# Kernel optimization log

Measured on AMD Instinct MI355X. Metric: run time of the kernel, lower is better.

## Reference

```python
import jax, jax.numpy as jnp
import numpy as np

B, T, C = 2, 2048, 2048
H, KVH, HD = 16, 4, 128  # heads, kv heads, head_dim
G = H // KVH             # GQA group size
THETA = 10000.0


def _rope_cos_sin(t, hd, dtype):
    inv_freq = 1.0 / (THETA ** (jnp.arange(0, hd, 2, dtype=jnp.float32) / hd))
    pos = jnp.arange(t, dtype=jnp.float32)
    freqs = pos[:, None] * inv_freq[None, :]          # [T, hd/2]
    emb = jnp.concatenate([freqs, freqs], axis=-1)    # [T, hd]
    return jnp.cos(emb).astype(dtype), jnp.sin(emb).astype(dtype)


def _rotate_half(x):
    x1, x2 = jnp.split(x, 2, axis=-1)
    return jnp.concatenate([-x2, x1], axis=-1)


def setup_inputs() -> dict:
    key = jax.random.key(0)
    ks = jax.random.split(key, 5)
    s_in = 1.0 / np.sqrt(C)
    return {
        "x": jax.random.normal(ks[0], (B, T, C), jnp.float32),
        "wq": jax.random.normal(ks[1], (C, H * HD), jnp.float32) * s_in,
        "bq": jnp.zeros((H * HD,), jnp.float32),
        "wk": jax.random.normal(ks[2], (C, KVH * HD), jnp.float32) * s_in,
        "bk": jnp.zeros((KVH * HD,), jnp.float32),
        "wv": jax.random.normal(ks[3], (C, KVH * HD), jnp.float32) * s_in,
        "bv": jnp.zeros((KVH * HD,), jnp.float32),
        "wo": jax.random.normal(ks[4], (H * HD, C), jnp.float32) * (1.0 / np.sqrt(H * HD)),
    }


def reference(x, wq, bq, wk, bk, wv, bv, wo):
    b, t, c = x.shape
    q = (x @ wq + bq).reshape(b, t, H, HD).transpose(0, 2, 1, 3)    # [B,H,T,hd]
    k = (x @ wk + bk).reshape(b, t, KVH, HD).transpose(0, 2, 1, 3)  # [B,KVH,T,hd]
    v = (x @ wv + bv).reshape(b, t, KVH, HD).transpose(0, 2, 1, 3)

    cos, sin = _rope_cos_sin(t, HD, x.dtype)  # [T,hd]
    q = q * cos + _rotate_half(q) * sin
    k = k * cos + _rotate_half(k) * sin

    # GQA: group query heads over kv heads
    qg = q.reshape(b, KVH, G, t, HD)
    scale = 1.0 / np.sqrt(HD)
    scores = jnp.einsum('bkgtd,bksd->bkgts', qg, k) * scale  # [B,KVH,G,T,T]
    causal = jnp.tril(jnp.ones((t, t), bool))
    scores = jnp.where(causal, scores, jnp.finfo(scores.dtype).min)
    attn = jax.nn.softmax(scores, axis=-1)
    out = jnp.einsum('bkgts,bksd->bkgtd', attn, v)            # [B,KVH,G,T,hd]
    out = out.reshape(b, H, t, HD).transpose(0, 2, 1, 3).reshape(b, t, H * HD)
    return out @ wo
```

## Files before the change

### kernel.cpp

```cpp
#include <hip/hip_runtime.h>
#include <hip/hip_bf16.h>
#include <math.h>

#define B_ 2
#define T_ 2048
#define C_ 2048
#define H_ 16
#define KVH_ 4
#define HD_ 128
#define G_ (H_ / KVH_)
#define MROWS (B_ * T_)
#define NQKV (H_ * HD_ + 2 * KVH_ * HD_)
#define KOFF (H_ * HD_)
#define VOFF (H_ * HD_ + KVH_ * HD_)
#define L2T (13.287712379549449f / 64.0f)

typedef __hip_bfloat16 bf16;
typedef short bf16x8 __attribute__((ext_vector_type(8)));
typedef short bf16x4 __attribute__((ext_vector_type(4)));
typedef float f32x4 __attribute__((ext_vector_type(4)));

__device__ __forceinline__ void gload_lds16(const void* g, void* l) {
  __builtin_amdgcn_global_load_lds(
      (const __attribute__((address_space(1))) unsigned int*)g,
      (__attribute__((address_space(3))) unsigned int*)l, 16, 0, 0);
}

static __device__ __forceinline__ f32x4 mfma32k(bf16x8 a, bf16x8 b, f32x4 c) {
  return __builtin_amdgcn_mfma_f32_16x16x32_bf16(a, b, c, 0, 0, 0);
}

static __device__ __forceinline__ f32x4 mfma16(bf16x4 a, bf16x4 b, f32x4 c) {
#if __has_builtin(__builtin_amdgcn_mfma_f32_16x16x16_bf16)
  return __builtin_amdgcn_mfma_f32_16x16x16_bf16(a, b, c, 0, 0, 0);
#else
  return __builtin_amdgcn_mfma_f32_16x16x16bf16_1k(a, b, c, 0, 0, 0);
#endif
}

static __device__ __forceinline__ short f2bf(float x) {
  unsigned u = __builtin_bit_cast(unsigned, x);
  u += 0x7FFFu + ((u >> 16) & 1u);
  return (short)(u >> 16);
}

static __device__ __forceinline__ float bfh2f(short h) {
  unsigned u = ((unsigned)(unsigned short)h) << 16;
  return __builtin_bit_cast(float, u);
}

static __device__ __forceinline__ float fexp2(float x) {
#if __has_builtin(__builtin_amdgcn_exp2f)
  return __builtin_amdgcn_exp2f(x);
#else
  return exp2f(x);
#endif
}

__global__ __launch_bounds__(256) void prep_kernel(
    const float* __restrict__ x, bf16* __restrict__ xb,
    const float* __restrict__ wq, const float* __restrict__ wk,
    const float* __restrict__ wv, bf16* __restrict__ wqkvT,
    const float* __restrict__ wo, bf16* __restrict__ woT,
    float2* __restrict__ tab) {
  __shared__ float t[32][33];
  int bid = blockIdx.x;
  if (bid < 8192) {
    const int i = (bid * 256 + threadIdx.x) * 4;
    float4 v = *(const float4*)(x + i);
    xb[i + 0] = __float2bfloat16(v.x);
    xb[i + 1] = __float2bfloat16(v.y);
    xb[i + 2] = __float2bfloat16(v.z);
    xb[i + 3] = __float2bfloat16(v.w);
    return;
  }
  bid -= 8192;
  if (bid < 6144) {
    const int tx = threadIdx.x & 31, ty = threadIdx.x >> 5;
    const int c0 = (bid % 96) * 32;
    const int r0 = (bid / 96) * 32;
    const float* src;
    int nn, ld;
    if (c0 < KOFF)      { src = wq; nn = c0;        ld = 2048; }
    else if (c0 < VOFF) { src = wk; nn = c0 - KOFF; ld = 512; }
    else                { src = wv; nn = c0 - VOFF; ld = 512; }
#pragma unroll
    for (int it = 0; it < 4; ++it)
      t[ty + 8 * it][tx] = src[(size_t)(r0 + ty + 8 * it) * ld + nn + tx];
    __syncthreads();
#pragma unroll
    for (int it = 0; it < 4; ++it)
      wqkvT[(size_t)(c0 + ty + 8 * it) * 2048 + r0 + tx] =
          __float2bfloat16(t[tx][ty + 8 * it]);
    return;
  }
  bid -= 6144;
  if (bid < 4096) {
    const int tx = threadIdx.x & 31, ty = threadIdx.x >> 5;
    const int c0 = (bid & 63) * 32;
    const int r0 = (bid >> 6) * 32;
#pragma unroll
    for (int it = 0; it < 4; ++it)
      t[ty + 8 * it][tx] = wo[(size_t)(r0 + ty + 8 * it) * 2048 + c0 + tx];
    __syncthreads();
#pragma unroll
    for (int it = 0; it < 4; ++it)
      woT[(size_t)(c0 + ty + 8 * it) * 2048 + r0 + tx] =
          __float2bfloat16(t[tx][ty + 8 * it]);
    return;
  }
  bid -= 4096;
  {
    const int idx = bid * 256 + threadIdx.x;
    const int tt = idx >> 6, i = idx & 63;
    const float invf = fexp2(-(float)i * L2T);
    float s, c;
    __sincosf((float)tt * invf, &s, &c);
    tab[idx] = make_float2(c, s);
  }
}

__global__ __launch_bounds__(256) void pack_kv(const bf16* __restrict__ qkv,
                                               bf16* __restrict__ kp,
                                               bf16* __restrict__ vp,
                                               const float2* __restrict__ tab) {
  const int pid = blockIdx.x;
  if (pid < 512) {
    const int tile = pid & 63;
    const int bk = pid >> 6;
    const int b = bk >> 2, kvh = bk & 3;
#pragma unroll
    for (int u = 0; u < 2; ++u) {
      const int t = threadIdx.x + u * 256;
      const int kc = t >> 6, L = t & 63;
      const int trow = tile * 32 + 16 * (kc >> 2) + (L & 15);
      const bf16* src = qkv + (size_t)(b * T_ + trow) * NQKV +
                        KOFF + kvh * HD_ + (kc & 3) * 32 + (L >> 4) * 8;
      bf16x8 vs = *(const bf16x8*)src;
      bf16x8 vpair = *(const bf16x8*)(src + (((kc & 2) == 0) ? 64 : -64));
      const float2* tp = tab + trow * 64 + (kc & 1) * 32 + (L >> 4) * 8;
      bf16x8 outv;
#pragma unroll
      for (int jj = 0; jj < 8; ++jj) {
        const float2 cs = tp[jj];
        const float a = bfh2f(vs[jj]), p = bfh2f(vpair[jj]);
        outv[jj] = f2bf(((kc & 2) == 0) ? (a * cs.x - p * cs.y)
                                        : (a * cs.x + p * cs.y));
      }
      *(bf16x8*)(kp + ((size_t)(bk * 64 + tile) * 8 + kc) * 512 + L * 8) = outv;
    }
    return;
  }
  {
    const int pid2 = pid - 512;
    const int tile = pid2 & 63;
    const int bk = pid2 >> 6;
    const int b = bk >> 2, kvh = bk & 3;
#pragma unroll
    for (int u = 0; u < 2; ++u) {
      const int t = threadIdx.x + u * 256;
      const int ht = t >> 6, L = t & 63;
      const int colL = L & 15, quad = L >> 4;
      const bf16* base = qkv + (size_t)(b * T_ + tile * 32 + quad * 4) * NQKV +
                         VOFF + kvh * HD_ + ht * 16 + colL;
      bf16x8 v;
#pragma unroll
      for (int jj = 0; jj < 4; ++jj) {
        v[jj]     = *(const short*)(base + (size_t)jj * NQKV);
        v[jj + 4] = *(const short*)(base + (size_t)(16 + jj) * NQKV);
      }
      *(bf16x8*)(vp + ((size_t)(bk * 64 + tile) * 8 + ht) * 512 + L * 8) = v;
    }
  }
}

template <bool BF16OUT>
__global__ __launch_bounds__(256, 2) void gemm_mfma(
    const bf16* __restrict__ A, const bf16* __restrict__ Bt, void* __restrict__ Cout,
    const float* __restrict__ bq, const float* __restrict__ bk2,
    const float* __restrict__ bv2, int M, int N, int K) {
  __shared__ __align__(16) bf16 As[128 * 32];
  __shared__ __align__(16) bf16 Bs[128 * 32];
  const int tid = threadIdx.x;
  const int w = tid >> 6, lane = tid & 63;
  const int colL = lane & 15, quad = lane >> 4;
  const int wm = w & 1, wn = w >> 1;
  const int r0 = blockIdx.y * 128, c0 = blockIdx.x * 128;

  f32x4 acc[4][4];
  const f32x4 zero = {0.f, 0.f, 0.f, 0.f};
#pragma unroll
  for (int mt = 0; mt < 4; ++mt)
#pragma unroll
    for (int nt = 0; nt < 4; ++nt) acc[mt][nt] = zero;

  for (int k0 = 0; k0 < K; k0 += 32) {
    __syncthreads();
#pragma unroll
    for (int it = 0; it < 2; ++it) {
      const int seg = it * 4 + w;
      const int idx = seg * 64 + lane;
      const int row = idx >> 2, off = idx & 3;
      gload_lds16(A + (size_t)(r0 + row) * K + k0 + off * 8, &As[seg * 512]);
      gload_lds16(Bt + (size_t)(c0 + row) * K + k0 + off * 8, &Bs[seg * 512]);
    }
    __syncthreads();
    bf16x8 af[4], bfv[4];
#pragma unroll
    for (int mt = 0; mt < 4; ++mt)
      af[mt] = *(const bf16x8*)&As[(wm * 64 + mt * 16 + colL) * 32 + quad * 8];
#pragma unroll
    for (int nt = 0; nt < 4; ++nt)
      bfv[nt] = *(const bf16x8*)&Bs[(wn * 64 + nt * 16 + colL) * 32 + quad * 8];
#pragma unroll
    for (int mt = 0; mt < 4; ++mt)
#pragma unroll
      for (int nt = 0; nt < 4; ++nt)
        acc[mt][nt] =
            __builtin_amdgcn_mfma_f32_16x16x32_bf16(af[mt], bfv[nt], acc[mt][nt], 0, 0, 0);
  }

#pragma unroll
  for (int nt = 0; nt < 4; ++nt) {
    const int c = c0 + wn * 64 + nt * 16 + colL;
    float bias = 0.f;
    if (bq) bias = (c < KOFF) ? bq[c] : (c < VOFF ? bk2[c - KOFF] : bv2[c - VOFF]);
#pragma unroll
    for (int mt = 0; mt < 4; ++mt) {
#pragma unroll
      for (int i = 0; i < 4; ++i) {
        const int r = r0 + wm * 64 + mt * 16 + quad * 4 + i;
        const float v = acc[mt][nt][i] + bias;
        if (BF16OUT)
          ((bf16*)Cout)[(size_t)r * N + c] = __float2bfloat16(v);
        else
          ((float*)Cout)[(size_t)r * N + c] = v;
      }
    }
  }
}

#define FA_SCL2 (0.08838834764831845f * 1.4426950408889634f)
#define FA_M2 16.0f

__global__ __launch_bounds__(256, 3) void flash_mfma8(
    const bf16* __restrict__ qkv, const bf16* __restrict__ kp,
    const bf16* __restrict__ vp, bf16* __restrict__ ao,
    const float2* __restrict__ tab) {
  __shared__ __align__(16) bf16 KS[3][4096];
  __shared__ __align__(16) bf16 VS[3][4096];

  const int id = blockIdx.x;
  const int bk = id & 7;
  const int u = id >> 3;
  const int jq = 127 - u;
  const int b = bk >> 2, kvh = bk & 3;
  const int w = threadIdx.x >> 6;
  const int h = (kvh << 2) | w;
  const int lane = threadIdx.x & 63;
  const int colL = lane & 15, quad = lane >> 4;
  const int myq0 = jq * 16;
  const int nkv = (jq >> 1) + 1;

  const bf16* kpt = kp + ((size_t)(bk * 64)) * 4096 + (w * 2) * 512 + lane * 8;
  const bf16* vpt = vp + ((size_t)(bk * 64)) * 4096 + (w * 2) * 512 + lane * 8;

  auto stageK = [&](int tile, int slot) {
    const bf16* s = kpt + (size_t)tile * 4096;
    bf16* d = &KS[slot][(w * 2) * 512];
    gload_lds16(s, d);
    gload_lds16(s + 512, d + 512);
  };
  auto stageV = [&](int tile, int slot) {
    const bf16* s = vpt + (size_t)tile * 4096;
    bf16* d = &VS[slot][(w * 2) * 512];
    gload_lds16(s, d);
    gload_lds16(s + 512, d + 512);
  };

  bf16x8 qf[4];
  {
    const bf16* qg = qkv + (size_t)(b * T_ + myq0) * NQKV + h * HD_;
    bf16x8 rq[4];
#pragma unroll
    for (int c = 0; c < 4; ++c)
      rq[c] = *(const bf16x8*)(qg + (size_t)colL * NQKV + c * 32 + quad * 8);
    const float2* tp = tab + (myq0 + colL) * 64 + quad * 8;
    float2 cs0[8], cs1[8];
#pragma unroll
    for (int jj = 0; jj < 8; ++jj) { cs0[jj] = tp[jj]; cs1[jj] = tp[32 + jj]; }
#pragma unroll
    for (int c = 0; c < 4; ++c) {
#pragma unroll
      for (int jj = 0; jj < 8; ++jj) {
        const float2 cs = (c & 1) ? cs1[jj] : cs0[jj];
        const float a = bfh2f(rq[c][jj]), p = bfh2f(rq[c ^ 2][jj]);
        qf[c][jj] = f2bf((c & 2) ? (a * cs.x + p * cs.y)
                                 : (a * cs.x - p * cs.y));
      }
    }
  }

  const f32x4 zero = {0.f, 0.f, 0.f, 0.f};
  auto qk = [&](const bf16* Kb, f32x4 (&s_)[2]) {
    s_[0] = zero; s_[1] = zero;
#pragma unroll
    for (int c = 0; c < 4; ++c) {
      bf16x8 kf0 = *(const bf16x8*)(Kb + c * 512 + lane * 8);
      bf16x8 kf1 = *(const bf16x8*)(Kb + (4 + c) * 512 + lane * 8);
      s_[0] = mfma32k(kf0, qf[c], s_[0]);
      s_[1] = mfma32k(kf1, qf[c], s_[1]);
    }
  };

  f32x4 o[8];
#pragma unroll
  for (int ht = 0; ht < 8; ++ht) o[ht] = zero;
  float l_ = 0.f;

  stageK(0, 0);
  if (nkv > 1) stageK(1, 1);
  if (nkv > 2) stageK(2, 2);
  stageV(0, 0);
  if (nkv > 1) stageV(1, 1);
  asm volatile("s_waitcnt vmcnt(0)\n\ts_barrier" ::: "memory");

  f32x4 sA[2], sB[2];
  qk(KS[0], sA);

  int kStage = 0, kNext = 1, vRead = 0, vStage = 2;
#pragma unroll 1
  for (int tt = 0; tt < nkv; ++tt) {
    const bool sk = (tt + 3 < nkv), sv = (tt + 2 < nkv);
    if (sk) stageK(tt + 3, kStage);
    if (sv) stageV(tt + 2, vStage);

    if (tt + 1 < nkv) qk(KS[kNext], sB);

    bf16x4 pf[2];
    if (tt == nkv - 1) {
      const int qg = ((jq & 1) << 4) | colL;
#pragma unroll
      for (int kt = 0; kt < 2; ++kt) {
        const int kb = kt * 16 + quad * 4;
        float pv[4];
#pragma unroll
        for (int i = 0; i < 4; ++i) {
          float e = fexp2(fmaf(sA[kt][i], FA_SCL2, -FA_M2));
          pv[i] = (kb + i <= qg) ? e : 0.f;
        }
        l_ += (pv[0] + pv[1]) + (pv[2] + pv[3]);
        pf[kt] = (bf16x4){f2bf(pv[0]), f2bf(pv[1]), f2bf(pv[2]), f2bf(pv[3])};
      }
    } else {
#pragma unroll
      for (int kt = 0; kt < 2; ++kt) {
        float pv[4];
#pragma unroll
        for (int i = 0; i < 4; ++i)
          pv[i] = fexp2(fmaf(sA[kt][i], FA_SCL2, -FA_M2));
        l_ += (pv[0] + pv[1]) + (pv[2] + pv[3]);
        pf[kt] = (bf16x4){f2bf(pv[0]), f2bf(pv[1]), f2bf(pv[2]), f2bf(pv[3])};
      }
    }

    {
      const bf16* Vb = VS[vRead];
#pragma unroll
      for (int ht = 0; ht < 8; ++ht) {
        bf16x8 vf8 = *(const bf16x8*)(Vb + ht * 512 + lane * 8);
        bf16x4 lo = __builtin_shufflevector(vf8, vf8, 0, 1, 2, 3);
        bf16x4 hi = __builtin_shufflevector(vf8, vf8, 4, 5, 6, 7);
        o[ht] = mfma16(lo, pf[0], o[ht]);
        o[ht] = mfma16(hi, pf[1], o[ht]);
      }
    }

    if (sk)      asm volatile("s_waitcnt vmcnt(4)\n\ts_barrier" ::: "memory");
    else if (sv) asm volatile("s_waitcnt vmcnt(2)\n\ts_barrier" ::: "memory");
    else         asm volatile("s_waitcnt vmcnt(0)\n\ts_barrier" ::: "memory");

    sA[0] = sB[0]; sA[1] = sB[1];
    kStage = (kStage == 2) ? 0 : kStage + 1;
    kNext  = (kNext == 2) ? 0 : kNext + 1;
    vRead  = (vRead == 2) ? 0 : vRead + 1;
    vStage = (vStage == 2) ? 0 : vStage + 1;
  }

  {
    float lv = l_;
    lv += __shfl_xor(lv, 16);
    lv += __shfl_xor(lv, 32);
    const float rl = 1.f / lv;
    const size_t rbase = (size_t)(b * T_ + myq0 + colL) * (H_ * HD_) + h * HD_;
#pragma unroll
    for (int ht = 0; ht < 8; ++ht) {
      bf16x4 ov;
#pragma unroll
      for (int i = 0; i < 4; ++i) ov[i] = f2bf(o[ht][i] * rl);
      *(bf16x4*)(ao + rbase + ht * 16 + quad * 4) = ov;
    }
  }
}

extern "C" void kernel_launch(void* const* d_in, const int* in_sizes, int n_in,
                              void* d_out, int out_size, void* d_ws, size_t ws_size,
                              hipStream_t stream) {
  (void)in_sizes; (void)n_in; (void)out_size; (void)ws_size;
  const float* x  = (const float*)d_in[0];
  const float* wq = (const float*)d_in[1];
  const float* bq = (const float*)d_in[2];
  const float* wk = (const float*)d_in[3];
  const float* bk = (const float*)d_in[4];
  const float* wv = (const float*)d_in[5];
  const float* bv = (const float*)d_in[6];
  const float* wo = (const float*)d_in[7];
  float* out = (float*)d_out;

  char* ws = (char*)d_ws;
  bf16* xb    = (bf16*)ws;
  bf16* wqkvT = (bf16*)(ws + (16u << 20));
  bf16* woT   = (bf16*)(ws + (28u << 20));
  bf16* qkv   = (bf16*)(ws + (36u << 20));
  bf16* kp    = (bf16*)(ws + (60u << 20));
  bf16* vp    = (bf16*)(ws + (68u << 20));
  float2* tab = (float2*)(ws + (76u << 20));

  prep_kernel<<<dim3(18944), dim3(256), 0, stream>>>(
      x, xb, wq, wk, wv, wqkvT, wo, woT, tab);

  gemm_mfma<true><<<dim3(NQKV / 128, MROWS / 128), dim3(256), 0, stream>>>(
      xb, wqkvT, qkv, bq, bk, bv, MROWS, NQKV, C_);

  pack_kv<<<dim3(1024), dim3(256), 0, stream>>>(qkv, kp, vp, tab);

  bf16* ao = xb;
  flash_mfma8<<<dim3(1024), dim3(256), 0, stream>>>(qkv, kp, vp, ao, tab);

  gemm_mfma<false><<<dim3(C_ / 128, MROWS / 128), dim3(256), 0, stream>>>(
      ao, woT, out, nullptr, nullptr, nullptr, MROWS, C_, KOFF);
}
```

Measured before the change: 308.8 us.

## Use K=32 MFMA for PV and shrink V buffering to raise occupancy

```diff
diff --git a/kernel.cpp b/kernel.cpp
--- a/kernel.cpp
+++ b/kernel.cpp
@@ -28,14 +28,6 @@
 
 static __device__ __forceinline__ f32x4 mfma32k(bf16x8 a, bf16x8 b, f32x4 c) {
   return __builtin_amdgcn_mfma_f32_16x16x32_bf16(a, b, c, 0, 0, 0);
-}
-
-static __device__ __forceinline__ f32x4 mfma16(bf16x4 a, bf16x4 b, f32x4 c) {
-#if __has_builtin(__builtin_amdgcn_mfma_f32_16x16x16_bf16)
-  return __builtin_amdgcn_mfma_f32_16x16x16_bf16(a, b, c, 0, 0, 0);
-#else
-  return __builtin_amdgcn_mfma_f32_16x16x16bf16_1k(a, b, c, 0, 0, 0);
-#endif
 }
 
 static __device__ __forceinline__ short f2bf(float x) {
@@ -133,7 +125,7 @@
     for (int u = 0; u < 2; ++u) {
       const int t = threadIdx.x + u * 256;
       const int kc = t >> 6, L = t & 63;
-      const int trow = tile * 32 + 16 * (kc >> 2) + (L & 15);
+      const int trow = tile * 32 + ((L >> 2) & 3) * 8 + (kc >> 2) * 4 + (L & 3);
       const bf16* src = qkv + (size_t)(b * T_ + trow) * NQKV +
                         KOFF + kvh * HD_ + (kc & 3) * 32 + (L >> 4) * 8;
       bf16x8 vs = *(const bf16x8*)src;
@@ -161,14 +153,12 @@
       const int t = threadIdx.x + u * 256;
       const int ht = t >> 6, L = t & 63;
       const int colL = L & 15, quad = L >> 4;
-      const bf16* base = qkv + (size_t)(b * T_ + tile * 32 + quad * 4) * NQKV +
+      const bf16* base = qkv + (size_t)(b * T_ + tile * 32 + quad * 8) * NQKV +
                          VOFF + kvh * HD_ + ht * 16 + colL;
       bf16x8 v;
 #pragma unroll
-      for (int jj = 0; jj < 4; ++jj) {
-        v[jj]     = *(const short*)(base + (size_t)jj * NQKV);
-        v[jj + 4] = *(const short*)(base + (size_t)(16 + jj) * NQKV);
-      }
+      for (int jj = 0; jj < 8; ++jj)
+        v[jj] = *(const short*)(base + (size_t)jj * NQKV);
       *(bf16x8*)(vp + ((size_t)(bk * 64 + tile) * 8 + ht) * 512 + L * 8) = v;
     }
   }
@@ -243,12 +233,12 @@
 #define FA_SCL2 (0.08838834764831845f * 1.4426950408889634f)
 #define FA_M2 16.0f
 
-__global__ __launch_bounds__(256, 3) void flash_mfma8(
+__global__ __launch_bounds__(256, 4) void flash_mfma8(
     const bf16* __restrict__ qkv, const bf16* __restrict__ kp,
     const bf16* __restrict__ vp, bf16* __restrict__ ao,
     const float2* __restrict__ tab) {
   __shared__ __align__(16) bf16 KS[3][4096];
-  __shared__ __align__(16) bf16 VS[3][4096];
+  __shared__ __align__(16) bf16 VS[2][4096];
 
   const int id = blockIdx.x;
   const int bk = id & 7;
@@ -322,27 +312,26 @@
   if (nkv > 1) stageK(1, 1);
   if (nkv > 2) stageK(2, 2);
   stageV(0, 0);
-  if (nkv > 1) stageV(1, 1);
   asm volatile("s_waitcnt vmcnt(0)\n\ts_barrier" ::: "memory");
 
   f32x4 sA[2], sB[2];
   qk(KS[0], sA);
 
-  int kStage = 0, kNext = 1, vRead = 0, vStage = 2;
+  int kStage = 0, kNext = 1;
 #pragma unroll 1
   for (int tt = 0; tt < nkv; ++tt) {
-    const bool sk = (tt + 3 < nkv), sv = (tt + 2 < nkv);
+    const bool sv = (tt + 1 < nkv), sk = (tt + 3 < nkv);
+    if (sv) stageV(tt + 1, (tt + 1) & 1);
     if (sk) stageK(tt + 3, kStage);
-    if (sv) stageV(tt + 2, vStage);
-
-    if (tt + 1 < nkv) qk(KS[kNext], sB);
+
+    if (sv) qk(KS[kNext], sB);
 
     bf16x4 pf[2];
     if (tt == nkv - 1) {
       const int qg = ((jq & 1) << 4) | colL;
 #pragma unroll
       for (int kt = 0; kt < 2; ++kt) {
-        const int kb = kt * 16 + quad * 4;
+        const int kb = quad * 8 + kt * 4;
         float pv[4];
 #pragma unroll
         for (int i = 0; i < 4; ++i) {
@@ -365,26 +354,21 @@
     }
 
     {
-      const bf16* Vb = VS[vRead];
+      const bf16* Vb = VS[tt & 1];
+      const bf16x8 pcat = __builtin_shufflevector(pf[0], pf[1], 0, 1, 2, 3, 4, 5, 6, 7);
 #pragma unroll
       for (int ht = 0; ht < 8; ++ht) {
         bf16x8 vf8 = *(const bf16x8*)(Vb + ht * 512 + lane * 8);
-        bf16x4 lo = __builtin_shufflevector(vf8, vf8, 0, 1, 2, 3);
-        bf16x4 hi = __builtin_shufflevector(vf8, vf8, 4, 5, 6, 7);
-        o[ht] = mfma16(lo, pf[0], o[ht]);
-        o[ht] = mfma16(hi, pf[1], o[ht]);
-      }
-    }
-
-    if (sk)      asm volatile("s_waitcnt vmcnt(4)\n\ts_barrier" ::: "memory");
-    else if (sv) asm volatile("s_waitcnt vmcnt(2)\n\ts_barrier" ::: "memory");
-    else         asm volatile("s_waitcnt vmcnt(0)\n\ts_barrier" ::: "memory");
+        o[ht] = mfma32k(vf8, pcat, o[ht]);
+      }
+    }
+
+    if (sk) asm volatile("s_waitcnt vmcnt(2)\n\ts_barrier" ::: "memory");
+    else    asm volatile("s_waitcnt vmcnt(0)\n\ts_barrier" ::: "memory");
 
     sA[0] = sB[0]; sA[1] = sB[1];
     kStage = (kStage == 2) ? 0 : kStage + 1;
     kNext  = (kNext == 2) ? 0 : kNext + 1;
-    vRead  = (vRead == 2) ? 0 : vRead + 1;
-    vStage = (vStage == 2) ? 0 : vStage + 1;
   }
 
   {
```

Result: no change. 303.9 us (-1.6%).
